# Performance work log

Measured on AMD Instinct MI355X. Metric: run time of the kernel, lower is better.

Reference implementation:

```python
import jax, jax.numpy as jnp
import numpy as np

ALPHAS = (0.1, 0.3, 0.5)
WEIGHTS = (0.5, 0.3, 0.2)

B, T, D = 32, 8192, 64


def setup_inputs() -> dict:
    key = jax.random.key(0)
    k1, k2 = jax.random.split(key)
    pred = jax.random.normal(k1, (B, T, D), dtype=jnp.float32)
    target = jax.random.normal(k2, (B, T, D), dtype=jnp.float32)
    return {"pred": pred, "target": target}


def _ema(x, alpha):
    # ema_0 = x_0 ; ema_i = alpha*x_i + (1-alpha)*ema_{i-1}
    # Express each step as affine op (mult, add) and compose with an
    # associative scan along the time axis (dim=1):  y_i = mult*y_{i-1} + add.
    mult = jnp.full(x.shape, 1.0 - alpha, dtype=x.dtype).at[:, 0].set(0.0)
    add = (alpha * x).at[:, 0].set(x[:, 0])

    def combine(c1, c2):  # apply c1 first, then c2
        a1, b1 = c1
        a2, b2 = c2
        return (a1 * a2, b1 * a2 + b2)

    _, ema = jax.lax.associative_scan(combine, (mult, add), axis=1)
    return ema


def _scale_loss(pred, target, alpha):
    pe = _ema(pred, alpha)   # [B, T, D]
    te = _ema(target, alpha)
    pd = pe[:, 1:] - pe[:, :-1]
    td = te[:, 1:] - te[:, :-1]
    mismatch = jnp.sign(pd) != jnp.sign(td)
    step_err = jnp.square(pe[:, 1:] - te[:, 1:])
    masked = jnp.where(mismatch, step_err, jnp.zeros_like(step_err))
    return masked.mean(axis=1)  # [B, D]


def reference(pred, target):
    loss = sum(w * _scale_loss(pred, target, a) for a, w in zip(ALPHAS, WEIGHTS))
    return loss.mean()  # reduction='mean'
```

## Files before the change

kernel.cpp:

```cpp
#include <hip/hip_runtime.h>


namespace {
constexpr int BB  = 32;
constexpr int TT  = 8192;
constexpr int DD  = 64;
constexpr int CH  = 32;
constexpr int WU  = 32;
constexpr int NCH = TT / CH;
constexpr int WPB = 4;
constexpr int BT  = 16;
constexpr float INV_NORM = 1.0f / (8191.0f * 2048.0f);
}

__global__ void zero_out_kernel(float* o) { o[0] = 0.0f; }

__device__ __forceinline__ void step1(float xx, float yy, float a, float wg,
                                      float& pe, float& te, float& acc) {
  float dx = xx - pe;
  float dy = yy - te;
  pe = fmaf(a, dx, pe);
  te = fmaf(a, dy, te);
  float e   = pe - te;
  float sel = (dx * dy < 0.0f) ? wg : 0.0f;
  acc = fmaf(sel, e * e, acc);
}

__global__ __launch_bounds__(256, 8) void ms_trend_loss_kernel(
    const float* __restrict__ pred, const float* __restrict__ targ,
    float* __restrict__ out) {
  const int lane = threadIdx.x & 63;
  const int wave = threadIdx.x >> 6;
  const int unit = blockIdx.x * WPB + wave;
  const int b = unit >> 8;
  const int c = unit & 255;
  const int s = c * CH;
  const int start = (c == 0) ? 0 : (s - WU);
  const int nw    = s - start;
  const int total = nw + CH;

  const float* p = pred + (b * TT + start) * DD + lane;
  const float* q = targ + (b * TT + start) * DD + lane;

  float pe0, pe1, pe2, te0, te1, te2;
  float acc = 0.0f;
  float xs[BT], ys[BT];

#pragma unroll
  for (int i = 0; i < BT; ++i) {
    xs[i] = p[i * DD];
    ys[i] = q[i * DD];
  }
  pe0 = pe1 = pe2 = xs[0];
  te0 = te1 = te2 = ys[0];
  {
    const float g = (nw == 0) ? 1.0f : 0.0f;
    const float w0 = 0.5f * g, w1 = 0.3f * g, w2 = 0.2f * g;
#pragma unroll
    for (int i = 0; i < BT; ++i) {
      step1(xs[i], ys[i], 0.1f, w0, pe0, te0, acc);
      step1(xs[i], ys[i], 0.3f, w1, pe1, te1, acc);
      step1(xs[i], ys[i], 0.5f, w2, pe2, te2, acc);
    }
  }

  for (int bt = BT; bt < total; bt += BT) {
#pragma unroll
    for (int i = 0; i < BT; ++i) {
      xs[i] = p[(bt + i) * DD];
      ys[i] = q[(bt + i) * DD];
    }
    const float g = (bt >= nw) ? 1.0f : 0.0f;
    const float w0 = 0.5f * g, w1 = 0.3f * g, w2 = 0.2f * g;
#pragma unroll
    for (int i = 0; i < BT; ++i) {
      step1(xs[i], ys[i], 0.1f, w0, pe0, te0, acc);
      step1(xs[i], ys[i], 0.3f, w1, pe1, te1, acc);
      step1(xs[i], ys[i], 0.5f, w2, pe2, te2, acc);
    }
  }

#pragma unroll
  for (int off = 32; off > 0; off >>= 1) acc += __shfl_down(acc, off);
  __shared__ float sred[WPB];
  if (lane == 0) sred[wave] = acc;
  __syncthreads();
  if (threadIdx.x == 0) {
    float t = sred[0] + sred[1] + sred[2] + sred[3];
    atomicAdd(out, t * INV_NORM);
  }
}

extern "C" void kernel_launch(void* const* d_in, const int* in_sizes, int n_in,
                              void* d_out, int out_size, void* d_ws, size_t ws_size,
                              hipStream_t stream) {
  (void)in_sizes; (void)n_in; (void)out_size; (void)d_ws; (void)ws_size;
  const float* pred = (const float*)d_in[0];
  const float* targ = (const float*)d_in[1];
  float* out = (float*)d_out;

  zero_out_kernel<<<1, 1, 0, stream>>>(out);
  ms_trend_loss_kernel<<<BB * NCH / WPB, 256, 0, stream>>>(pred, targ, out);
}
```

Baseline: 154.7 us.

## Vectorize loads to float4 with quarter-wave chunks and double-buffered prefetch

Each wave now handles four time chunks, one per 16-lane quarter, and each lane loads a float4 covering four feature columns, so it keeps three EMA states per column. Loads are double-buffered in two register batches, so the next batch is fetched while the current one is computed. The aim is wider memory transactions, fewer blocks, and load latency hidden behind the EMA arithmetic. In exchange register use per thread rises (occupancy hint lowered to 4) and the chunk's first 32-step warm-up window is still recomputed.

```diff
diff --git a/kernel.cpp b/kernel.cpp
--- a/kernel.cpp
+++ b/kernel.cpp
@@ -6,77 +6,97 @@
 constexpr int TT  = 8192;
 constexpr int DD  = 64;
 constexpr int CH  = 32;
-constexpr int WU  = 32;
 constexpr int NCH = TT / CH;
 constexpr int WPB = 4;
-constexpr int BT  = 16;
+constexpr int NSTEP = 64;
+constexpr int BT  = 4;
+constexpr int NB  = NSTEP / BT;
 constexpr float INV_NORM = 1.0f / (8191.0f * 2048.0f);
 }
 
 __global__ void zero_out_kernel(float* o) { o[0] = 0.0f; }
 
-__device__ __forceinline__ void step1(float xx, float yy, float a, float wg,
+__device__ __forceinline__ void load_batch(const float4* __restrict__ p4,
+                                           const float4* __restrict__ q4,
+                                           int kb, float4 (&xs)[BT], float4 (&ys)[BT]) {
+#pragma unroll
+  for (int i = 0; i < BT; ++i) {
+    xs[i] = p4[(kb * BT + i) * 16];
+    ys[i] = q4[(kb * BT + i) * 16];
+  }
+}
+
+__device__ __forceinline__ void stepc(float xx, float yy, float a, float w,
                                       float& pe, float& te, float& acc) {
   float dx = xx - pe;
   float dy = yy - te;
   pe = fmaf(a, dx, pe);
   te = fmaf(a, dy, te);
   float e   = pe - te;
-  float sel = (dx * dy < 0.0f) ? wg : 0.0f;
+  float sel = (dx * dy < 0.0f) ? w : 0.0f;
   acc = fmaf(sel, e * e, acc);
 }
 
-__global__ __launch_bounds__(256, 8) void ms_trend_loss_kernel(
+__device__ __forceinline__ void comp_batch(const float4 (&xs)[BT], const float4 (&ys)[BT],
+    float w0, float w1, float w2,
+    float (&pe)[3][4], float (&te)[3][4], float& acc) {
+#pragma unroll
+  for (int i = 0; i < BT; ++i) {
+    const float xv[4] = {xs[i].x, xs[i].y, xs[i].z, xs[i].w};
+    const float yv[4] = {ys[i].x, ys[i].y, ys[i].z, ys[i].w};
+#pragma unroll
+    for (int k = 0; k < 4; ++k) {
+      stepc(xv[k], yv[k], 0.1f, w0, pe[0][k], te[0][k], acc);
+      stepc(xv[k], yv[k], 0.3f, w1, pe[1][k], te[1][k], acc);
+      stepc(xv[k], yv[k], 0.5f, w2, pe[2][k], te[2][k], acc);
+    }
+  }
+}
+
+__global__ __launch_bounds__(256, 4) void ms_trend_loss_kernel(
     const float* __restrict__ pred, const float* __restrict__ targ,
     float* __restrict__ out) {
   const int lane = threadIdx.x & 63;
   const int wave = threadIdx.x >> 6;
+  const int li   = lane & 15;
+  const int qt   = lane >> 4;
   const int unit = blockIdx.x * WPB + wave;
-  const int b = unit >> 8;
-  const int c = unit & 255;
-  const int s = c * CH;
-  const int start = (c == 0) ? 0 : (s - WU);
-  const int nw    = s - start;
-  const int total = nw + CH;
+  const int b    = unit >> 6;
+  const int g    = unit & 63;
+  const int c    = g * 4 + qt;
+  const int start = (c == 0) ? 0 : (c - 1) * CH;
+  const int lo    = (c == 0) ? 0 : 32;
+  const int hi    = (c == 0) ? 32 : 64;
 
-  const float* p = pred + (b * TT + start) * DD + lane;
-  const float* q = targ + (b * TT + start) * DD + lane;
+  const float4* p4 = (const float4*)(pred + ((size_t)b * TT + start) * DD) + li;
+  const float4* q4 = (const float4*)(targ + ((size_t)b * TT + start) * DD) + li;
 
-  float pe0, pe1, pe2, te0, te1, te2;
+  float4 xa[BT], ya[BT], xb[BT], yb[BT];
+  load_batch(p4, q4, 0, xa, ya);
+  load_batch(p4, q4, 1, xb, yb);
+
+  float pe[3][4], te[3][4];
+  {
+    const float xv[4] = {xa[0].x, xa[0].y, xa[0].z, xa[0].w};
+    const float yv[4] = {ya[0].x, ya[0].y, ya[0].z, ya[0].w};
+#pragma unroll
+    for (int j = 0; j < 3; ++j)
+#pragma unroll
+      for (int k = 0; k < 4; ++k) { pe[j][k] = xv[k]; te[j][k] = yv[k]; }
+  }
   float acc = 0.0f;
-  float xs[BT], ys[BT];
 
 #pragma unroll
-  for (int i = 0; i < BT; ++i) {
-    xs[i] = p[i * DD];
-    ys[i] = q[i * DD];
-  }
-  pe0 = pe1 = pe2 = xs[0];
-  te0 = te1 = te2 = ys[0];
-  {
-    const float g = (nw == 0) ? 1.0f : 0.0f;
-    const float w0 = 0.5f * g, w1 = 0.3f * g, w2 = 0.2f * g;
-#pragma unroll
-    for (int i = 0; i < BT; ++i) {
-      step1(xs[i], ys[i], 0.1f, w0, pe0, te0, acc);
-      step1(xs[i], ys[i], 0.3f, w1, pe1, te1, acc);
-      step1(xs[i], ys[i], 0.5f, w2, pe2, te2, acc);
-    }
-  }
-
-  for (int bt = BT; bt < total; bt += BT) {
-#pragma unroll
-    for (int i = 0; i < BT; ++i) {
-      xs[i] = p[(bt + i) * DD];
-      ys[i] = q[(bt + i) * DD];
-    }
-    const float g = (bt >= nw) ? 1.0f : 0.0f;
-    const float w0 = 0.5f * g, w1 = 0.3f * g, w2 = 0.2f * g;
-#pragma unroll
-    for (int i = 0; i < BT; ++i) {
-      step1(xs[i], ys[i], 0.1f, w0, pe0, te0, acc);
-      step1(xs[i], ys[i], 0.3f, w1, pe1, te1, acc);
-      step1(xs[i], ys[i], 0.5f, w2, pe2, te2, acc);
+  for (int kb = 0; kb < NB; ++kb) {
+    const int t0 = kb * BT;
+    const float gf = (t0 >= lo && t0 < hi) ? 1.0f : 0.0f;
+    const float w0 = 0.5f * gf, w1 = 0.3f * gf, w2 = 0.2f * gf;
+    if ((kb & 1) == 0) {
+      comp_batch(xa, ya, w0, w1, w2, pe, te, acc);
+      if (kb + 2 < NB) load_batch(p4, q4, kb + 2, xa, ya);
+    } else {
+      comp_batch(xb, yb, w0, w1, w2, pe, te, acc);
+      if (kb + 2 < NB) load_batch(p4, q4, kb + 2, xb, yb);
     }
   }
 
@@ -100,5 +120,5 @@
   float* out = (float*)d_out;
 
   zero_out_kernel<<<1, 1, 0, stream>>>(out);
-  ms_trend_loss_kernel<<<BB * NCH / WPB, 256, 0, stream>>>(pred, targ, out);
+  ms_trend_loss_kernel<<<BB * NCH / (4 * WPB), 256, 0, stream>>>(pred, targ, out);
 }
```

After: 158.4 us. +2.4%, slower.
